# Optimization experiments

Hardware: AMD Instinct MI355X
Metric: run time of the kernel (lower is better)

Reference implementation:

```python
import jax, jax.numpy as jnp
import numpy as np


def setup_inputs() -> dict:
    key = jax.random.key(0)
    ks = jax.random.split(key, 5)
    B, D, T, H = 32, 256, 1024, 512
    s = 1.0 / np.sqrt(H)  # PyTorch default init scale
    return {
        "x": jax.random.normal(ks[0], (B, D, T), dtype=jnp.float32),
        "W_ih": jax.random.uniform(ks[1], (4 * H, D), jnp.float32, -s, s),
        "W_hh": jax.random.uniform(ks[2], (4 * H, H), jnp.float32, -s, s),
        "b_ih": jax.random.uniform(ks[3], (4 * H,), jnp.float32, -s, s),
        "b_hh": jax.random.uniform(ks[4], (4 * H,), jnp.float32, -s, s),
    }


def reference(x, W_ih, W_hh, b_ih, b_hh):
    # x: [B, in_dim, T] -> permute to [B, T, in_dim] as in the torch module
    B, D, T = x.shape
    H = W_hh.shape[1]
    xt = jnp.transpose(x, (0, 2, 1))  # [B, T, D]
    # Precompute input contribution for all timesteps in one GEMM: [B, T, 4H]
    gx_all = jnp.einsum("btd,gd->btg", xt, W_ih) + b_ih + b_hh
    gx_all = jnp.swapaxes(gx_all, 0, 1)  # [T, B, 4H] for scan

    def step(carry, gx):
        h, c = carry
        g = gx + h @ W_hh.T  # [B, 4H]
        i, f, gg, o = jnp.split(g, 4, axis=-1)  # PyTorch gate order i,f,g,o
        i = jax.nn.sigmoid(i)
        f = jax.nn.sigmoid(f)
        gg = jnp.tanh(gg)
        o = jax.nn.sigmoid(o)
        c = f * c + i * gg
        h = o * jnp.tanh(c)
        return (h, c), h

    h0 = jnp.zeros((B, H), dtype=x.dtype)
    c0 = jnp.zeros((B, H), dtype=x.dtype)
    _, hs = jax.lax.scan(step, (h0, c0), gx_all)  # hs: [T, B, H]
    out = jnp.transpose(hs, (1, 2, 0))  # [B, H, T] (return_sequences=True)
    return out
```

## Files before the change

kernel.cpp:

```cpp
#include <hip/hip_runtime.h>
#include <math.h>


using short8 = __attribute__((ext_vector_type(8))) short;
using f32x4  = __attribute__((ext_vector_type(4))) float;
using float4v = __attribute__((ext_vector_type(4))) float;

__device__ inline unsigned short f2bf(float f) {
    unsigned u = __float_as_uint(f);
    unsigned r = u + 0x7fffu + ((u >> 16) & 1u);
    return (unsigned short)(r >> 16);
}
__device__ inline float fsig(float x) {
    return __builtin_amdgcn_rcpf(1.0f + __expf(-x));
}
__device__ inline float ftanh(float x) {
    return 2.0f * __builtin_amdgcn_rcpf(1.0f + __expf(-2.0f * x)) - 1.0f;
}

__global__ void zero_flags(unsigned* p) {
    p[blockIdx.x * 256 + threadIdx.x] = 0u;
}

__global__ __launch_bounds__(256) void x_transpose(const float* __restrict__ x,
                                                   unsigned short* __restrict__ xT) {
    __shared__ unsigned short tile[64][65];
    const int tid = threadIdx.x;
    const int t0 = blockIdx.x * 64, d0 = blockIdx.y * 64, b = blockIdx.z;
    for (int p = 0; p < 16; p++) {
        int d = p * 4 + (tid >> 6);
        int t = tid & 63;
        tile[d][t] = f2bf(x[(b * 256 + d0 + d) * 1024 + t0 + t]);
    }
    __syncthreads();
    for (int p = 0; p < 16; p++) {
        int t = p * 4 + (tid >> 6);
        int d = tid & 63;
        xT[(size_t)(t0 + t) * 8192 + b * 256 + d0 + d] = tile[d][t];
    }
}

#define HS 520
#define XS 264
#define GS 33
#define OS 17

__global__ __launch_bounds__(512) void lstm_rec(const unsigned short* __restrict__ xT,
                                                const float* __restrict__ Wih,
                                                const float* __restrict__ Whh,
                                                const float* __restrict__ bih,
                                                const float* __restrict__ bhh,
                                                float* __restrict__ out,
                                                unsigned* flags,
                                                unsigned* hbuf_dw) {
    __shared__ __align__(16) unsigned short h_lds[16 * HS];
    __shared__ __align__(16) unsigned short x_lds[2][16 * XS];
    __shared__ float gates_lds[4 * 16 * GS];
    __shared__ __align__(8) unsigned short hstage[512];
    __shared__ float out_stage[512 * OS];

    const int tid  = threadIdx.x;
    const int wave = tid >> 6;
    const int lane = tid & 63;
    const int quad = lane >> 4, l15 = lane & 15;
    const int group = blockIdx.x & 1;
    const int g     = blockIdx.x >> 1;
    const int gate  = wave >> 1;
    const int csub  = (wave & 1) * 16;

    const int nrow = gate * 512 + g * 32 + csub + l15;

    short8 whh_frag[16];
    for (int ks = 0; ks < 16; ks++) {
        const float* p = &Whh[(size_t)nrow * 512 + ks * 32 + quad * 8];
        short8 v;
        for (int j = 0; j < 8; j++) v[j] = (short)f2bf(p[j]);
        whh_frag[ks] = v;
    }
    short8 wih_frag[8];
    for (int ks = 0; ks < 8; ks++) {
        const float* p = &Wih[(size_t)nrow * 256 + ks * 32 + quad * 8];
        short8 v;
        for (int j = 0; j < 8; j++) v[j] = (short)f2bf(p[j]);
        wih_frag[ks] = v;
    }
    const float bias_n = bih[nrow] + bhh[nrow];

    for (int i = tid; i < 16 * HS; i += 512) h_lds[i] = 0;
    {
        const unsigned short* src = xT + (size_t)(group * 16 + (tid >> 5)) * 256 + (tid & 31) * 8;
        *(short8*)&x_lds[0][(tid >> 5) * XS + (tid & 31) * 8] = *(const short8*)src;
    }

    const int eb = tid >> 5, ek = tid & 31;
    const int hidx = g * 32 + ek;
    float c = 0.0f;
    float* out_base = out + ((size_t)(group * 16 + eb) * 512 + hidx) * 1024;
    unsigned* my_flags = flags + group * 512;
    unsigned* hb_base = hbuf_dw + group * 8192;

    __syncthreads();

    f32x4 accA = f32x4{bias_n, bias_n, bias_n, bias_n};
    f32x4 accB = f32x4{0.f, 0.f, 0.f, 0.f};
    for (int ks = 0; ks < 8; ks += 2) {
        short8 a0 = *(const short8*)&x_lds[0][l15 * XS + ks * 32 + quad * 8];
        short8 a1 = *(const short8*)&x_lds[0][l15 * XS + (ks + 1) * 32 + quad * 8];
        accA = __builtin_amdgcn_mfma_f32_16x16x32_bf16(a0, wih_frag[ks], accA, 0, 0, 0);
        accB = __builtin_amdgcn_mfma_f32_16x16x32_bf16(a1, wih_frag[ks + 1], accB, 0, 0, 0);
    }

    for (int t = 0; t < 1024; t++) {
        for (int ks = 0; ks < 16; ks += 2) {
            short8 a0 = *(const short8*)&h_lds[l15 * HS + ks * 32 + quad * 8];
            short8 a1 = *(const short8*)&h_lds[l15 * HS + (ks + 1) * 32 + quad * 8];
            accA = __builtin_amdgcn_mfma_f32_16x16x32_bf16(a0, whh_frag[ks], accA, 0, 0, 0);
            accB = __builtin_amdgcn_mfma_f32_16x16x32_bf16(a1, whh_frag[ks + 1], accB, 0, 0, 0);
        }
        for (int r = 0; r < 4; r++) {
            int b = quad * 4 + r;
            gates_lds[(gate * 16 + b) * GS + csub + l15] = accA[r] + accB[r];
        }

        if (t + 1 < 1024) {
            const unsigned short* src = xT + (size_t)(t + 1) * 8192 +
                                        (size_t)(group * 16 + eb) * 256 + ek * 8;
            *(short8*)&x_lds[(t + 1) & 1][eb * XS + ek * 8] = *(const short8*)src;
        }
        __syncthreads();

        float iv = gates_lds[(0 * 16 + eb) * GS + ek];
        float fv = gates_lds[(1 * 16 + eb) * GS + ek];
        float gv = gates_lds[(2 * 16 + eb) * GS + ek];
        float ov = gates_lds[(3 * 16 + eb) * GS + ek];
        iv = fsig(iv); fv = fsig(fv); gv = ftanh(gv); ov = fsig(ov);
        c = fv * c + iv * gv;
        float h = ov * ftanh(c);

        out_stage[tid * OS + (t & 15)] = h;
        hstage[eb * 32 + ek] = f2bf(h);
        __syncthreads();

        if (t < 1023) {
            if (tid < 256) {
                unsigned v = *(const unsigned*)&hstage[tid * 2];
                int b = tid >> 4, cp = tid & 15;
                __hip_atomic_store(&hb_base[(t & 1) * 4096 + b * 256 + g * 16 + cp], v,
                                   __ATOMIC_RELAXED, __HIP_MEMORY_SCOPE_AGENT);
            }
            __builtin_amdgcn_s_waitcnt(0);
            __syncthreads();
            if (tid == 0)
                __hip_atomic_store(&my_flags[g * 32], (unsigned)(t + 1),
                                   __ATOMIC_RELAXED, __HIP_MEMORY_SCOPE_AGENT);
        }

        if ((t & 15) == 15) {
            int t0 = t & ~15;
            for (int q = 0; q < 4; q++) {
                float4v v = *(const float4v*)&out_stage[tid * OS + q * 4];
                *(float4v*)&out_base[t0 + q * 4] = v;
            }
        }

        if (t == 1023) break;

        accA = f32x4{bias_n, bias_n, bias_n, bias_n};
        accB = f32x4{0.f, 0.f, 0.f, 0.f};
        {
            const unsigned short* xb = x_lds[(t + 1) & 1];
            for (int ks = 0; ks < 8; ks += 2) {
                short8 a0 = *(const short8*)&xb[l15 * XS + ks * 32 + quad * 8];
                short8 a1 = *(const short8*)&xb[l15 * XS + (ks + 1) * 32 + quad * 8];
                accA = __builtin_amdgcn_mfma_f32_16x16x32_bf16(a0, wih_frag[ks], accA, 0, 0, 0);
                accB = __builtin_amdgcn_mfma_f32_16x16x32_bf16(a1, wih_frag[ks + 1], accB, 0, 0, 0);
            }
        }

        if (wave == 0 && lane < 16) {
            while (__hip_atomic_load(&my_flags[lane * 32], __ATOMIC_RELAXED,
                                     __HIP_MEMORY_SCOPE_AGENT) <= (unsigned)t) { }
        }
        __syncthreads();

        {
            const unsigned long long* src =
                (const unsigned long long*)&hb_base[(t & 1) * 4096 + eb * 256 + ek * 8];
            unsigned long long v0 = __hip_atomic_load(src + 0, __ATOMIC_RELAXED, __HIP_MEMORY_SCOPE_AGENT);
            unsigned long long v1 = __hip_atomic_load(src + 1, __ATOMIC_RELAXED, __HIP_MEMORY_SCOPE_AGENT);
            unsigned long long v2 = __hip_atomic_load(src + 2, __ATOMIC_RELAXED, __HIP_MEMORY_SCOPE_AGENT);
            unsigned long long v3 = __hip_atomic_load(src + 3, __ATOMIC_RELAXED, __HIP_MEMORY_SCOPE_AGENT);
            unsigned long long* dst = (unsigned long long*)&h_lds[eb * HS + ek * 16];
            dst[0] = v0; dst[1] = v1; dst[2] = v2; dst[3] = v3;
        }
        __syncthreads();
    }
}

extern "C" void kernel_launch(void* const* d_in, const int* in_sizes, int n_in,
                              void* d_out, int out_size, void* d_ws, size_t ws_size,
                              hipStream_t stream) {
    (void)in_sizes; (void)n_in; (void)out_size; (void)ws_size;
    const float* x   = (const float*)d_in[0];
    const float* Wih = (const float*)d_in[1];
    const float* Whh = (const float*)d_in[2];
    const float* bih = (const float*)d_in[3];
    const float* bhh = (const float*)d_in[4];
    float* out = (float*)d_out;

    char* ws = (char*)d_ws;
    unsigned short* xT = (unsigned short*)ws;
    unsigned* flags    = (unsigned*)(ws + 16777216);
    unsigned* hbuf_dw  = (unsigned*)(ws + 16777216 + 8192);

    zero_flags<<<8, 256, 0, stream>>>(flags);
    dim3 gT(16, 4, 32);
    x_transpose<<<gT, 256, 0, stream>>>(x, xT);
    lstm_rec<<<32, 512, 0, stream>>>(xT, Wih, Whh, bih, bhh, out, flags, hbuf_dw);
}
```

Measured before the change: 3.137 ms.

## Replace flag handshake with step-tagged 64-bit h words in LSTM exchange

Each thread now publishes its bf16 hidden pair together with the timestep in the upper 32 bits of a 64-bit word. Consumers spin on these tags directly, which removes the separate flag array, the LDS staging buffer, two block barriers per step and the zero_flags launch. A block's own columns are written straight into LDS instead of going round-trip through global memory. The risk is that the workspace is never cleared, so stale words from an earlier run that carry a matching tag could be consumed, and every thread now does its own polling.

After: 3.322 ms. +5.9%, slower.

```diff
diff --git a/kernel.cpp b/kernel.cpp
--- a/kernel.cpp
+++ b/kernel.cpp
@@ -2,9 +2,10 @@
 #include <math.h>
 
 
-using short8 = __attribute__((ext_vector_type(8))) short;
-using f32x4  = __attribute__((ext_vector_type(4))) float;
+using short8  = __attribute__((ext_vector_type(8))) short;
+using f32x4   = __attribute__((ext_vector_type(4))) float;
 using float4v = __attribute__((ext_vector_type(4))) float;
+using uint4v  = __attribute__((ext_vector_type(4))) unsigned;
 
 __device__ inline unsigned short f2bf(float f) {
     unsigned u = __float_as_uint(f);
@@ -16,10 +17,6 @@
 }
 __device__ inline float ftanh(float x) {
     return 2.0f * __builtin_amdgcn_rcpf(1.0f + __expf(-2.0f * x)) - 1.0f;
-}
-
-__global__ void zero_flags(unsigned* p) {
-    p[blockIdx.x * 256 + threadIdx.x] = 0u;
 }
 
 __global__ __launch_bounds__(256) void x_transpose(const float* __restrict__ x,
@@ -51,12 +48,10 @@
                                                 const float* __restrict__ bih,
                                                 const float* __restrict__ bhh,
                                                 float* __restrict__ out,
-                                                unsigned* flags,
-                                                unsigned* hbuf_dw) {
+                                                unsigned long long* hbuf) {
     __shared__ __align__(16) unsigned short h_lds[16 * HS];
     __shared__ __align__(16) unsigned short x_lds[2][16 * XS];
     __shared__ float gates_lds[4 * 16 * GS];
-    __shared__ __align__(8) unsigned short hstage[512];
     __shared__ float out_stage[512 * OS];
 
     const int tid  = threadIdx.x;
@@ -94,10 +89,10 @@
 
     const int eb = tid >> 5, ek = tid & 31;
     const int hidx = g * 32 + ek;
+    const bool self_cols = (ek >> 1) == g;
     float c = 0.0f;
     float* out_base = out + ((size_t)(group * 16 + eb) * 512 + hidx) * 1024;
-    unsigned* my_flags = flags + group * 512;
-    unsigned* hb_base = hbuf_dw + group * 8192;
+    unsigned long long* hb_row0 = hbuf + (size_t)(group * 16 + eb) * 256;
 
     __syncthreads();
 
@@ -138,21 +133,16 @@
         float h = ov * ftanh(c);
 
         out_stage[tid * OS + (t & 15)] = h;
-        hstage[eb * 32 + ek] = f2bf(h);
-        __syncthreads();
-
-        if (t < 1023) {
-            if (tid < 256) {
-                unsigned v = *(const unsigned*)&hstage[tid * 2];
-                int b = tid >> 4, cp = tid & 15;
-                __hip_atomic_store(&hb_base[(t & 1) * 4096 + b * 256 + g * 16 + cp], v,
-                                   __ATOMIC_RELAXED, __HIP_MEMORY_SCOPE_AGENT);
-            }
-            __builtin_amdgcn_s_waitcnt(0);
-            __syncthreads();
-            if (tid == 0)
-                __hip_atomic_store(&my_flags[g * 32], (unsigned)(t + 1),
-                                   __ATOMIC_RELAXED, __HIP_MEMORY_SCOPE_AGENT);
+
+        unsigned my = f2bf(h);
+        h_lds[eb * HS + hidx] = (unsigned short)my;
+
+        unsigned nb = (unsigned)__shfl_xor((int)my, 1);
+        if (t < 1023 && !(ek & 1)) {
+            unsigned long long v = ((unsigned long long)(unsigned)(t + 1) << 32) |
+                                   (unsigned long long)(my | (nb << 16));
+            __hip_atomic_store(&hb_row0[(size_t)(t & 1) * 8192 + g * 16 + (ek >> 1)], v,
+                               __ATOMIC_RELAXED, __HIP_MEMORY_SCOPE_AGENT);
         }
 
         if ((t & 15) == 15) {
@@ -177,21 +167,25 @@
             }
         }
 
-        if (wave == 0 && lane < 16) {
-            while (__hip_atomic_load(&my_flags[lane * 32], __ATOMIC_RELAXED,
-                                     __HIP_MEMORY_SCOPE_AGENT) <= (unsigned)t) { }
-        }
-        __syncthreads();
-
-        {
-            const unsigned long long* src =
-                (const unsigned long long*)&hb_base[(t & 1) * 4096 + eb * 256 + ek * 8];
-            unsigned long long v0 = __hip_atomic_load(src + 0, __ATOMIC_RELAXED, __HIP_MEMORY_SCOPE_AGENT);
-            unsigned long long v1 = __hip_atomic_load(src + 1, __ATOMIC_RELAXED, __HIP_MEMORY_SCOPE_AGENT);
-            unsigned long long v2 = __hip_atomic_load(src + 2, __ATOMIC_RELAXED, __HIP_MEMORY_SCOPE_AGENT);
-            unsigned long long v3 = __hip_atomic_load(src + 3, __ATOMIC_RELAXED, __HIP_MEMORY_SCOPE_AGENT);
-            unsigned long long* dst = (unsigned long long*)&h_lds[eb * HS + ek * 16];
-            dst[0] = v0; dst[1] = v1; dst[2] = v2; dst[3] = v3;
+        if (!self_cols) {
+            const unsigned long long* src = hb_row0 + (size_t)(t & 1) * 8192 + ek * 8;
+            unsigned long long v[8];
+            for (int j = 0; j < 8; j++)
+                v[j] = __hip_atomic_load(src + j, __ATOMIC_RELAXED, __HIP_MEMORY_SCOPE_AGENT);
+            const unsigned want = (unsigned)(t + 1);
+            bool again = true;
+            while (again) {
+                again = false;
+                for (int j = 0; j < 8; j++) {
+                    if ((unsigned)(v[j] >> 32) != want) {
+                        v[j] = __hip_atomic_load(src + j, __ATOMIC_RELAXED, __HIP_MEMORY_SCOPE_AGENT);
+                        again = true;
+                    }
+                }
+            }
+            uint4v* dst = (uint4v*)&h_lds[eb * HS + ek * 16];
+            dst[0] = uint4v{(unsigned)v[0], (unsigned)v[1], (unsigned)v[2], (unsigned)v[3]};
+            dst[1] = uint4v{(unsigned)v[4], (unsigned)v[5], (unsigned)v[6], (unsigned)v[7]};
         }
         __syncthreads();
     }
@@ -209,12 +203,10 @@
     float* out = (float*)d_out;
 
     char* ws = (char*)d_ws;
-    unsigned short* xT = (unsigned short*)ws;
-    unsigned* flags    = (unsigned*)(ws + 16777216);
-    unsigned* hbuf_dw  = (unsigned*)(ws + 16777216 + 8192);
-
-    zero_flags<<<8, 256, 0, stream>>>(flags);
+    unsigned short* xT      = (unsigned short*)ws;
+    unsigned long long* hbuf = (unsigned long long*)(ws + 16777216);
+
     dim3 gT(16, 4, 32);
     x_transpose<<<gT, 256, 0, stream>>>(x, xT);
-    lstm_rec<<<32, 512, 0, stream>>>(xT, Wih, Whh, bih, bhh, out, flags, hbuf_dw);
-}
+    lstm_rec<<<32, 512, 0, stream>>>(xT, Wih, Whh, bih, bhh, out, hbuf);
+}
```

## Split K across wave pairs, XOR-swizzle LDS, and publish h directly to shorten step critical path

Applied to the files above, without the earlier changes.

Each wave now handles both 16-column tiles over half of the K range, so an h fragment load feeds two MFMAs. Partial gate sums go to LDS and are added during the gate step. The padded LDS strides are replaced by an XOR swizzle to avoid bank conflicts. The hstage buffer and its extra barrier are removed: each thread writes its own h into local LDS and packs pairs via shuffle for the global store. The flag publish is moved after the next step's input-projection MFMAs, and a block skips reloading its own slice from global memory. The aim is to cut barriers and latency on the serial per-timestep path, at the cost of more complex indexing and a later flag release.

Measured after the change: 3.056 ms. 1.03x faster.

```diff
diff --git a/kernel.cpp b/kernel.cpp
--- a/kernel.cpp
+++ b/kernel.cpp
@@ -2,9 +2,10 @@
 #include <math.h>
 
 
-using short8 = __attribute__((ext_vector_type(8))) short;
-using f32x4  = __attribute__((ext_vector_type(4))) float;
+using short8  = __attribute__((ext_vector_type(8))) short;
+using f32x4   = __attribute__((ext_vector_type(4))) float;
 using float4v = __attribute__((ext_vector_type(4))) float;
+using uint4v  = __attribute__((ext_vector_type(4))) unsigned;
 
 __device__ inline unsigned short f2bf(float f) {
     unsigned u = __float_as_uint(f);
@@ -40,8 +41,6 @@
     }
 }
 
-#define HS 520
-#define XS 264
 #define GS 33
 #define OS 17
 
@@ -52,107 +51,108 @@
                                                 const float* __restrict__ bhh,
                                                 float* __restrict__ out,
                                                 unsigned* flags,
-                                                unsigned* hbuf_dw) {
-    __shared__ __align__(16) unsigned short h_lds[16 * HS];
-    __shared__ __align__(16) unsigned short x_lds[2][16 * XS];
-    __shared__ float gates_lds[4 * 16 * GS];
-    __shared__ __align__(8) unsigned short hstage[512];
+                                                unsigned* hbuf) {
+    __shared__ __align__(16) unsigned short h_lds[16 * 512];
+    __shared__ __align__(16) unsigned short x_lds[2][16 * 256];
+    __shared__ float gates_lds[8 * 16 * GS];
     __shared__ float out_stage[512 * OS];
 
     const int tid  = threadIdx.x;
     const int wave = tid >> 6;
     const int lane = tid & 63;
     const int quad = lane >> 4, l15 = lane & 15;
+    const int l7   = l15 & 7;
     const int group = blockIdx.x & 1;
     const int g     = blockIdx.x >> 1;
     const int gate  = wave >> 1;
-    const int csub  = (wave & 1) * 16;
-
-    const int nrow = gate * 512 + g * 32 + csub + l15;
-
-    short8 whh_frag[16];
-    for (int ks = 0; ks < 16; ks++) {
-        const float* p = &Whh[(size_t)nrow * 512 + ks * 32 + quad * 8];
-        short8 v;
-        for (int j = 0; j < 8; j++) v[j] = (short)f2bf(p[j]);
-        whh_frag[ks] = v;
-    }
-    short8 wih_frag[8];
-    for (int ks = 0; ks < 8; ks++) {
-        const float* p = &Wih[(size_t)nrow * 256 + ks * 32 + quad * 8];
-        short8 v;
-        for (int j = 0; j < 8; j++) v[j] = (short)f2bf(p[j]);
-        wih_frag[ks] = v;
-    }
-    const float bias_n = bih[nrow] + bhh[nrow];
-
-    for (int i = tid; i < 16 * HS; i += 512) h_lds[i] = 0;
+    const int kh    = wave & 1;
+
+    short8 whh_frag[2][8];
+    short8 wih_frag[2][4];
+    float bias_t[2];
+    for (int tile = 0; tile < 2; tile++) {
+        const int nrow = gate * 512 + g * 32 + tile * 16 + l15;
+        for (int ks = 0; ks < 8; ks++) {
+            const float* p = &Whh[(size_t)nrow * 512 + kh * 256 + ks * 32 + quad * 8];
+            short8 v;
+            for (int j = 0; j < 8; j++) v[j] = (short)f2bf(p[j]);
+            whh_frag[tile][ks] = v;
+        }
+        for (int ks = 0; ks < 4; ks++) {
+            const float* p = &Wih[(size_t)nrow * 256 + kh * 128 + ks * 32 + quad * 8];
+            short8 v;
+            for (int j = 0; j < 8; j++) v[j] = (short)f2bf(p[j]);
+            wih_frag[tile][ks] = v;
+        }
+        bias_t[tile] = (kh == 0) ? (bih[nrow] + bhh[nrow]) : 0.0f;
+    }
+
+    const int eb = tid >> 5, ek = tid & 31;
+    const int e7 = eb & 7;
+    const int hidx = g * 32 + ek;
+
+    for (int i = tid; i < 16 * 512; i += 512) h_lds[i] = 0;
     {
-        const unsigned short* src = xT + (size_t)(group * 16 + (tid >> 5)) * 256 + (tid & 31) * 8;
-        *(short8*)&x_lds[0][(tid >> 5) * XS + (tid & 31) * 8] = *(const short8*)src;
-    }
-
-    const int eb = tid >> 5, ek = tid & 31;
-    const int hidx = g * 32 + ek;
+        const unsigned short* src = xT + (size_t)(group * 16 + eb) * 256 + ek * 8;
+        *(short8*)&x_lds[0][eb * 256 + (ek ^ e7) * 8] = *(const short8*)src;
+    }
+
     float c = 0.0f;
     float* out_base = out + ((size_t)(group * 16 + eb) * 512 + hidx) * 1024;
     unsigned* my_flags = flags + group * 512;
-    unsigned* hb_base = hbuf_dw + group * 8192;
+    unsigned* hb_base  = hbuf + group * 8192;
 
     __syncthreads();
 
-    f32x4 accA = f32x4{bias_n, bias_n, bias_n, bias_n};
-    f32x4 accB = f32x4{0.f, 0.f, 0.f, 0.f};
-    for (int ks = 0; ks < 8; ks += 2) {
-        short8 a0 = *(const short8*)&x_lds[0][l15 * XS + ks * 32 + quad * 8];
-        short8 a1 = *(const short8*)&x_lds[0][l15 * XS + (ks + 1) * 32 + quad * 8];
-        accA = __builtin_amdgcn_mfma_f32_16x16x32_bf16(a0, wih_frag[ks], accA, 0, 0, 0);
-        accB = __builtin_amdgcn_mfma_f32_16x16x32_bf16(a1, wih_frag[ks + 1], accB, 0, 0, 0);
+    f32x4 acc0 = f32x4{bias_t[0], bias_t[0], bias_t[0], bias_t[0]};
+    f32x4 acc1 = f32x4{bias_t[1], bias_t[1], bias_t[1], bias_t[1]};
+    for (int ks = 0; ks < 4; ks++) {
+        short8 af = *(const short8*)&x_lds[0][l15 * 256 + (((kh << 4) + (ks << 2) + quad) ^ l7) * 8];
+        acc0 = __builtin_amdgcn_mfma_f32_16x16x32_bf16(af, wih_frag[0][ks], acc0, 0, 0, 0);
+        acc1 = __builtin_amdgcn_mfma_f32_16x16x32_bf16(af, wih_frag[1][ks], acc1, 0, 0, 0);
     }
 
     for (int t = 0; t < 1024; t++) {
-        for (int ks = 0; ks < 16; ks += 2) {
-            short8 a0 = *(const short8*)&h_lds[l15 * HS + ks * 32 + quad * 8];
-            short8 a1 = *(const short8*)&h_lds[l15 * HS + (ks + 1) * 32 + quad * 8];
-            accA = __builtin_amdgcn_mfma_f32_16x16x32_bf16(a0, whh_frag[ks], accA, 0, 0, 0);
-            accB = __builtin_amdgcn_mfma_f32_16x16x32_bf16(a1, whh_frag[ks + 1], accB, 0, 0, 0);
-        }
-        for (int r = 0; r < 4; r++) {
-            int b = quad * 4 + r;
-            gates_lds[(gate * 16 + b) * GS + csub + l15] = accA[r] + accB[r];
+        for (int ks = 0; ks < 8; ks++) {
+            short8 af = *(const short8*)&h_lds[l15 * 512 + (((kh << 5) + (ks << 2) + quad) ^ l7) * 8];
+            acc0 = __builtin_amdgcn_mfma_f32_16x16x32_bf16(af, whh_frag[0][ks], acc0, 0, 0, 0);
+            acc1 = __builtin_amdgcn_mfma_f32_16x16x32_bf16(af, whh_frag[1][ks], acc1, 0, 0, 0);
+        }
+        {
+            const int prow = (kh * 4 + gate) * 16;
+            for (int r = 0; r < 4; r++) {
+                gates_lds[(prow + quad * 4 + r) * GS + l15]      = acc0[r];
+                gates_lds[(prow + quad * 4 + r) * GS + 16 + l15] = acc1[r];
+            }
         }
 
         if (t + 1 < 1024) {
             const unsigned short* src = xT + (size_t)(t + 1) * 8192 +
                                         (size_t)(group * 16 + eb) * 256 + ek * 8;
-            *(short8*)&x_lds[(t + 1) & 1][eb * XS + ek * 8] = *(const short8*)src;
-        }
-        __syncthreads();
-
-        float iv = gates_lds[(0 * 16 + eb) * GS + ek];
-        float fv = gates_lds[(1 * 16 + eb) * GS + ek];
-        float gv = gates_lds[(2 * 16 + eb) * GS + ek];
-        float ov = gates_lds[(3 * 16 + eb) * GS + ek];
+            *(short8*)&x_lds[(t + 1) & 1][eb * 256 + (ek ^ e7) * 8] = *(const short8*)src;
+        }
+        __syncthreads();
+
+        float iv = gates_lds[(0 * 16 + eb) * GS + ek] + gates_lds[(4 * 16 + eb) * GS + ek];
+        float fv = gates_lds[(1 * 16 + eb) * GS + ek] + gates_lds[(5 * 16 + eb) * GS + ek];
+        float gv = gates_lds[(2 * 16 + eb) * GS + ek] + gates_lds[(6 * 16 + eb) * GS + ek];
+        float ov = gates_lds[(3 * 16 + eb) * GS + ek] + gates_lds[(7 * 16 + eb) * GS + ek];
         iv = fsig(iv); fv = fsig(fv); gv = ftanh(gv); ov = fsig(ov);
         c = fv * c + iv * gv;
         float h = ov * ftanh(c);
 
         out_stage[tid * OS + (t & 15)] = h;
-        hstage[eb * 32 + ek] = f2bf(h);
-        __syncthreads();
-
-        if (t < 1023) {
-            if (tid < 256) {
-                unsigned v = *(const unsigned*)&hstage[tid * 2];
-                int b = tid >> 4, cp = tid & 15;
-                __hip_atomic_store(&hb_base[(t & 1) * 4096 + b * 256 + g * 16 + cp], v,
-                                   __ATOMIC_RELAXED, __HIP_MEMORY_SCOPE_AGENT);
-            }
-            __builtin_amdgcn_s_waitcnt(0);
-            __syncthreads();
-            if (tid == 0)
-                __hip_atomic_store(&my_flags[g * 32], (unsigned)(t + 1),
-                                   __ATOMIC_RELAXED, __HIP_MEMORY_SCOPE_AGENT);
+
+        unsigned my = f2bf(h);
+        {
+            int phys = (g * 4 + (ek >> 3)) ^ e7;
+            h_lds[eb * 512 + phys * 8 + (ek & 7)] = (unsigned short)my;
+        }
+
+        unsigned nb = (unsigned)__shfl_xor((int)my, 1);
+        if (t < 1023 && !(ek & 1)) {
+            __hip_atomic_store(&hb_base[(t & 1) * 4096 + eb * 256 + g * 16 + (ek >> 1)],
+                               my | (nb << 16), __ATOMIC_RELAXED, __HIP_MEMORY_SCOPE_AGENT);
         }
 
         if ((t & 15) == 15) {
@@ -165,17 +165,22 @@
 
         if (t == 1023) break;
 
-        accA = f32x4{bias_n, bias_n, bias_n, bias_n};
-        accB = f32x4{0.f, 0.f, 0.f, 0.f};
+        acc0 = f32x4{bias_t[0], bias_t[0], bias_t[0], bias_t[0]};
+        acc1 = f32x4{bias_t[1], bias_t[1], bias_t[1], bias_t[1]};
         {
             const unsigned short* xb = x_lds[(t + 1) & 1];
-            for (int ks = 0; ks < 8; ks += 2) {
-                short8 a0 = *(const short8*)&xb[l15 * XS + ks * 32 + quad * 8];
-                short8 a1 = *(const short8*)&xb[l15 * XS + (ks + 1) * 32 + quad * 8];
-                accA = __builtin_amdgcn_mfma_f32_16x16x32_bf16(a0, wih_frag[ks], accA, 0, 0, 0);
-                accB = __builtin_amdgcn_mfma_f32_16x16x32_bf16(a1, wih_frag[ks + 1], accB, 0, 0, 0);
+            for (int ks = 0; ks < 4; ks++) {
+                short8 af = *(const short8*)&xb[l15 * 256 + (((kh << 4) + (ks << 2) + quad) ^ l7) * 8];
+                acc0 = __builtin_amdgcn_mfma_f32_16x16x32_bf16(af, wih_frag[0][ks], acc0, 0, 0, 0);
+                acc1 = __builtin_amdgcn_mfma_f32_16x16x32_bf16(af, wih_frag[1][ks], acc1, 0, 0, 0);
             }
         }
+
+        __builtin_amdgcn_s_waitcnt(0);
+        __syncthreads();
+        if (tid == 0)
+            __hip_atomic_store(&my_flags[g * 32], (unsigned)(t + 1),
+                               __ATOMIC_RELAXED, __HIP_MEMORY_SCOPE_AGENT);
 
         if (wave == 0 && lane < 16) {
             while (__hip_atomic_load(&my_flags[lane * 32], __ATOMIC_RELAXED,
@@ -183,15 +188,19 @@
         }
         __syncthreads();
 
-        {
+        if ((ek >> 1) != g) {
             const unsigned long long* src =
                 (const unsigned long long*)&hb_base[(t & 1) * 4096 + eb * 256 + ek * 8];
             unsigned long long v0 = __hip_atomic_load(src + 0, __ATOMIC_RELAXED, __HIP_MEMORY_SCOPE_AGENT);
             unsigned long long v1 = __hip_atomic_load(src + 1, __ATOMIC_RELAXED, __HIP_MEMORY_SCOPE_AGENT);
             unsigned long long v2 = __hip_atomic_load(src + 2, __ATOMIC_RELAXED, __HIP_MEMORY_SCOPE_AGENT);
             unsigned long long v3 = __hip_atomic_load(src + 3, __ATOMIC_RELAXED, __HIP_MEMORY_SCOPE_AGENT);
-            unsigned long long* dst = (unsigned long long*)&h_lds[eb * HS + ek * 16];
-            dst[0] = v0; dst[1] = v1; dst[2] = v2; dst[3] = v3;
+            int pa = (2 * ek) ^ e7;
+            int pb = (2 * ek + 1) ^ e7;
+            *(uint4v*)&h_lds[eb * 512 + pa * 8] =
+                uint4v{(unsigned)v0, (unsigned)(v0 >> 32), (unsigned)v1, (unsigned)(v1 >> 32)};
+            *(uint4v*)&h_lds[eb * 512 + pb * 8] =
+                uint4v{(unsigned)v2, (unsigned)(v2 >> 32), (unsigned)v3, (unsigned)(v3 >> 32)};
         }
         __syncthreads();
     }
@@ -211,10 +220,10 @@
     char* ws = (char*)d_ws;
     unsigned short* xT = (unsigned short*)ws;
     unsigned* flags    = (unsigned*)(ws + 16777216);
-    unsigned* hbuf_dw  = (unsigned*)(ws + 16777216 + 8192);
+    unsigned* hbuf     = (unsigned*)(ws + 16777216 + 8192);
 
     zero_flags<<<8, 256, 0, stream>>>(flags);
     dim3 gT(16, 4, 32);
     x_transpose<<<gT, 256, 0, stream>>>(x, xT);
-    lstm_rec<<<32, 512, 0, stream>>>(xT, Wih, Whh, bih, bhh, out, flags, hbuf_dw);
-}
+    lstm_rec<<<32, 512, 0, stream>>>(xT, Wih, Whh, bih, bhh, out, flags, hbuf);
+}
```
